# Kernel optimization log

Hardware: AMD Instinct MI355X
Metric: run time of the kernel (lower is better)

## Reference

```python
import jax, jax.numpy as jnp
import numpy as np

T = 16384  # sequence length (scan axis)
D = 512    # d_model


def setup_inputs() -> dict:
    key = jax.random.key(0)
    k1, k2, k3, k4 = jax.random.split(key, 4)
    inputs = jax.random.normal(k1, (T, D), dtype=jnp.float32)
    terminations = jax.random.bernoulli(k2, 0.01, (T,))
    c0 = jnp.zeros((D,), dtype=jnp.float32)
    h0 = jnp.zeros((D,), dtype=jnp.float32)
    # flax OptimizedLSTMCell fuses the 4 gates (order i, f, g, o) into one kernel
    scale = 1.0 / np.sqrt(D).astype(np.float32)
    Wx = jax.random.normal(k3, (D, 4 * D), dtype=jnp.float32) * scale  # input kernel (no bias in flax)
    Wh = jax.random.normal(k4, (D, 4 * D), dtype=jnp.float32) * scale  # recurrent kernel
    b = jnp.zeros((4 * D,), dtype=jnp.float32)                          # recurrent-dense bias
    return {"inputs": inputs, "terminations": terminations, "c0": c0, "h0": h0,
            "Wx": Wx, "Wh": Wh, "b": b}


def reference(inputs, terminations, c0, h0, Wx, Wh, b):
    def step(carry, xt):
        x, term = xt
        c, h = carry
        # reset_on_terminate: zero the carry when this step begins a new episode
        keep = jnp.where(term, jnp.zeros((), c.dtype), jnp.ones((), c.dtype))
        c = c * keep
        h = h * keep
        # fused gate pre-activations, flax gate order: i, f, g, o
        z = x @ Wx + h @ Wh + b  # [4*D]
        i, f, g, o = jnp.split(z, 4, axis=-1)
        new_c = jax.nn.sigmoid(f) * c + jax.nn.sigmoid(i) * jnp.tanh(g)
        new_h = jax.nn.sigmoid(o) * jnp.tanh(new_c)
        return (new_c, new_h), (new_c, new_h)

    _, (cs, hs) = jax.lax.scan(step, (c0, h0), (inputs, terminations))
    # original returns (y_t, new_states) with y_t == new_h per step -> (hs, (cs, hs))
    return hs, cs, hs
```

## Files before the change

kernel.cpp:

```cpp
#include <hip/hip_runtime.h>

typedef _Float16 half8 __attribute__((ext_vector_type(8)));
typedef float floatx4 __attribute__((ext_vector_type(4)));
typedef unsigned int u32x4 __attribute__((ext_vector_type(4)));
typedef unsigned long long u64;
typedef unsigned int u32;
typedef unsigned short u16;

#define T_LEN 16384
#define DM 512
#define NC 2048
#define NG 16
#define NR 16
#define WPG 16
#define WVG 32
#define PROBE_ROUNDS 12
#define PROBE_CAP 4000

struct Meta { int S; int use_h0; int steps_g[NG]; };

union FragU { u64 q[2]; u32x4 r; half8 v; };

__device__ __forceinline__ float sigf(float x) { return 1.0f / (1.0f + __expf(-x)); }
__device__ __forceinline__ float tanh_f(float x) { return 1.0f - 2.0f / (__expf(2.0f * x) + 1.0f); }

__global__ void zero_kernel(u32* __restrict__ p, size_t nwords) {
    size_t i = (size_t)blockIdx.x * blockDim.x + threadIdx.x;
    size_t stride = (size_t)gridDim.x * blockDim.x;
    for (; i < nwords; i += stride) p[i] = 0u;
}

__global__ void pack_f16_kernel(const float* __restrict__ src, _Float16* __restrict__ dst, int n8) {
    int i = blockIdx.x * blockDim.x + threadIdx.x;
    if (i >= n8) return;
    const floatx4* s = (const floatx4*)src + (size_t)i * 2;
    floatx4 a = s[0], b = s[1];
    half8 o;
    o[0] = (_Float16)a[0]; o[1] = (_Float16)a[1]; o[2] = (_Float16)a[2]; o[3] = (_Float16)a[3];
    o[4] = (_Float16)b[0]; o[5] = (_Float16)b[1]; o[6] = (_Float16)b[2]; o[7] = (_Float16)b[3];
    ((half8*)dst)[i] = o;
}

__global__ __launch_bounds__(256) void pack_w_kernel(const float* __restrict__ src, half8* __restrict__ dst) {
    int wid = blockIdx.x * 4 + (threadIdx.x >> 6);
    int l = threadIdx.x & 63;
    int tt = wid >> 4, kt = wid & 15;
    int q = tt & 3, cch = tt >> 2;
    int col = q * 512 + cch * 16 + (l & 15);
    int h = l >> 4;
    half8 o;
#pragma unroll
    for (int jj = 0; jj < 8; jj++) o[jj] = (_Float16)src[(size_t)(kt * 32 + h * 8 + jj) * NC + col];
    dst[(tt * 16 + kt) * 64 + l] = o;
}

__global__ void prep_kernel(const void* __restrict__ termraw, const float* __restrict__ h0,
                            int* __restrict__ seg_start, int* __restrict__ seg_len,
                            Meta* __restrict__ meta, _Float16* __restrict__ Hbuf) {
    __shared__ int cnts[256], offs[256];
    __shared__ int nzm, oddnz, totS;
    __shared__ int chain[256];
    int tid = threadIdx.x;
    if (tid == 0) { nzm = 0; oddnz = 0; }
    __syncthreads();
    const unsigned char* tb = (const unsigned char*)termraw;
    const int* ti = (const int*)termraw;
    int lm = 0;
    for (int i = tid; i < T_LEN; i += 256) {
        if (tb[i]) {
            int p = i & 3;
            if (p == 1 || p == 2) lm |= 1;
            else if (p == 3) lm |= 2;
            else lm |= 4;
        }
    }
    if (lm) atomicOr(&nzm, lm);
    __syncthreads();
    int mm = nzm;
    int bytemode = (mm & 1) ? 1 : 0;
    int floatmode = (!bytemode && (mm & 2)) ? 1 : 0;
    int lo = 0;
    if (!bytemode && !floatmode) {
        for (int k2 = 2 * tid + 1; k2 < T_LEN; k2 += 512) if (ti[k2]) lo = 1;
    }
    if (lo) atomicOr(&oddnz, 1);
    __syncthreads();
    int i64mode = (!bytemode && !floatmode && oddnz == 0 && (mm & 4)) ? 1 : 0;
    const float* tf = (const float*)termraw;

    auto termAt = [&](int t) -> int {
        if (bytemode) return tb[t] != 0;
        if (floatmode) return tf[t] != 0.0f;
        if (i64mode) return (ti[2 * t] != 0) || (ti[2 * t + 1] != 0);
        return ti[t] != 0;
    };

    int base = tid * 64;
    int cnt = 0;
    for (int k = 0; k < 64; k++) {
        int t = base + k;
        if (t == 0 || termAt(t)) cnt++;
    }
    cnts[tid] = cnt;
    __syncthreads();
    if (tid == 0) {
        int a = 0;
        for (int i = 0; i < 256; i++) { offs[i] = a; a += cnts[i]; }
        totS = a;
        meta->S = a;
    }
    __syncthreads();
    int S = totS;
    {
        int o = offs[tid];
        for (int k = 0; k < 64; k++) {
            int t = base + k;
            if (t == 0 || termAt(t)) seg_start[o++] = t;
        }
    }
    __syncthreads();
    for (int i = tid; i < S; i += 256)
        seg_len[i] = ((i + 1 < S) ? seg_start[i + 1] : T_LEN) - seg_start[i];
    __syncthreads();
    {
        int g = tid >> 4, r = tid & 15;
        int tot = 0;
        for (int i = g + 16 * r; i < S; i += 256) tot += seg_len[i];
        chain[tid] = tot;
    }
    __syncthreads();
    if (tid < NG) {
        int mx = 0;
        for (int r = 0; r < 16; r++) mx = max(mx, chain[tid * 16 + r]);
        meta->steps_g[tid] = mx;
    }
    int u = termAt(0);
    if (tid == 0) meta->use_h0 = !u;
    if (!u) {
        for (int d2 = tid; d2 < DM; d2 += 256)
            Hbuf[(d2 >> 3) * 128 + (d2 & 7)] = (_Float16)h0[d2];
    }
}

__global__ __launch_bounds__(256) void xw_gemm_kernel(const half8* __restrict__ A, const half8* __restrict__ B,
                                                      const float* __restrict__ bias, _Float16* __restrict__ XW) {
    int bx = blockIdx.x, by = blockIdx.y;
    int w = threadIdx.x >> 6, l = threadIdx.x & 63;
    int mbase = bx * 64 + w * 16;
    int h = l >> 4, n = l & 15;
    floatx4 acc[8] = {};
    int arow = mbase + n;
#pragma unroll
    for (int kt = 0; kt < 16; kt++) {
        half8 a = A[(size_t)arow * 64 + kt * 4 + h];
#pragma unroll
        for (int nt = 0; nt < 8; nt++)
            acc[nt] = __builtin_amdgcn_mfma_f32_16x16x32_f16(a, B[((by * 8 + nt) * 16 + kt) * 64 + l], acc[nt], 0, 0, 0);
    }
#pragma unroll
    for (int nt = 0; nt < 8; nt++) {
        int tt = by * 8 + nt, q = tt & 3, cch = tt >> 2;
        float bv = bias[q * 512 + cch * 16 + n];
#pragma unroll
        for (int r = 0; r < 4; r++) {
            int row = mbase + h * 4 + r;
            XW[(size_t)row * NC + tt * 16 + n] = (_Float16)(acc[nt][r] + bv);
        }
    }
}

struct Trk { int seg, t0, s0, end, active; };

__device__ __forceinline__ void trk_init(Trk& k, int row, int g, int S,
                                         const int* __restrict__ ss, const int* __restrict__ sl) {
    int seg = g + 16 * row;
    k.seg = seg;
    if (seg < S) { k.t0 = ss[seg]; k.s0 = 0; k.end = sl[seg]; k.active = 1; }
    else { k.t0 = 0; k.s0 = 0; k.end = 0x7fffffff; k.active = 0; }
}

__device__ __forceinline__ int trk_step(Trk& k, int s, int S,
                                        const int* __restrict__ ss, const int* __restrict__ sl, int& t_out) {
    int z = !k.active;
    if (s > 0 && k.active && s == k.end) {
        int seg = k.seg + 256;
        if (seg < S) { k.seg = seg; k.t0 = ss[seg]; k.s0 = s; k.end = s + sl[seg]; z = 1; }
        else { k.active = 0; z = 1; }
    }
    t_out = k.active ? (k.t0 + (s - k.s0)) : 0;
    return z;
}

template <bool L2C>
__device__ __forceinline__ void run_compute(
    const half8* __restrict__ PW, const _Float16* __restrict__ XW,
    const float* __restrict__ c0,
    const int* __restrict__ seg_start, const int* __restrict__ seg_len,
    u64* __restrict__ Hbuf, int* __restrict__ flags,
    int g, int jj, int w, int l, int steps, int S, int use_h0,
    u16 (&hstage)[2][NR][16], _Float16 (&xwstage)[2][NR][128],
    float (&outstage)[2][2][NR][32], int (&ioflag)[2], int (&outcnt)[2]) {
    const int c = jj * 2 + w;
    const int n = l & 15, h = l >> 4;
    const int d = c * 16 + n;
    const int m = n;

    half8 bf[4][16];
#pragma unroll
    for (int q = 0; q < 4; q++)
#pragma unroll
        for (int kt = 0; kt < 16; kt++) {
            bf[q][kt] = PW[((c * 4 + q) * 16 + kt) * 64 + l];
            asm volatile("" : "+v"(bf[q][kt]));
        }

    Trk trkM; trk_init(trkM, n, g, S, seg_start, seg_len);
    Trk trk[4];
#pragma unroll
    for (int r = 0; r < 4; r++) trk_init(trk[r], h * 4 + r, g, S, seg_start, seg_len);

    float cc[4];
#pragma unroll
    for (int r = 0; r < 4; r++) {
        int row = h * 4 + r;
        cc[r] = (g == 0 && row == 0 && use_h0) ? c0[d] : 0.0f;
    }

    FragU zu; zu.q[0] = 0; zu.q[1] = 0;
    const half8 zfrag = zu.v;

    int* fl = flags + g * WVG;
    const int wfid = jj * 2 + w;
    const int pollidx = l & 31;

    const int b2 = l >> 5, m2 = (l >> 1) & 15, half = l & 1;
    const int ktc = c >> 1, hhp = (c & 1) * 2 + b2;
    const int ldsIdx = m2 * 4 + b2 * 2 + half;
    const size_t hwIdx = (size_t)(ktc * 4 + hhp) * 32 + m2 * 2 + half;

    for (int s = 0; s < steps; ++s) {
        int tdump;
        const int zM = trk_step(trkM, s, S, seg_start, seg_len, tdump);
        int zz[4];
#pragma unroll
        for (int r = 0; r < 4; r++)
            zz[r] = trk_step(trk[r], s, S, seg_start, seg_len, tdump);

        while (__hip_atomic_load(&ioflag[s & 1], __ATOMIC_RELAXED, __HIP_MEMORY_SCOPE_WORKGROUP) < s)
            __builtin_amdgcn_s_sleep(1);
        asm volatile("" ::: "memory");
        float xwv[4][4];
#pragma unroll
        for (int q = 0; q < 4; q++)
#pragma unroll
            for (int r = 0; r < 4; r++)
                xwv[q][r] = (float)xwstage[s & 1][h * 4 + r][w * 64 + q * 16 + n];

        if (s > 0) {
            if constexpr (L2C) {
                const int* flp = &fl[pollidx];
                while (true) {
                    int v;
                    asm volatile("global_load_dword %0, %1, off sc0" : "=v"(v) : "v"(flp) : "memory");
                    asm volatile("s_waitcnt vmcnt(0)" ::: "memory");
                    if (__all(v >= s)) break;
                    __builtin_amdgcn_s_sleep(1);
                }
                asm volatile("" ::: "memory");
            } else {
                while (true) {
                    int v = __hip_atomic_load(&fl[pollidx], __ATOMIC_RELAXED, __HIP_MEMORY_SCOPE_AGENT);
                    if (__all(v >= s)) break;
                    __builtin_amdgcn_s_sleep(1);
                }
                asm volatile("" ::: "memory");
            }
        }

        const int rp = s & 1;
        u64* Hr = Hbuf + (size_t)(g * 2 + rp) * (NR * DM / 4);
        u64* Hw = Hbuf + (size_t)(g * 2 + (rp ^ 1)) * (NR * DM / 4);

        u32x4 raw[16];
#pragma unroll
        for (int kt = 0; kt < 16; kt++) {
            const void* ap = (const char*)Hr + (((size_t)kt * 64 + h * 16 + m) << 4);
            if constexpr (L2C)
                asm volatile("global_load_dwordx4 %0, %1, off sc0" : "=v"(raw[kt]) : "v"(ap) : "memory");
            else
                asm volatile("global_load_dwordx4 %0, %1, off sc1" : "=v"(raw[kt]) : "v"(ap) : "memory");
        }
        asm volatile("s_waitcnt vmcnt(0)" ::: "memory");
        __builtin_amdgcn_sched_barrier(0);
        half8 afr[16];
#pragma unroll
        for (int kt = 0; kt < 16; kt++) {
            FragU u; u.r = raw[kt];
            afr[kt] = zM ? zfrag : u.v;
        }

        floatx4 acc[4] = {};
#pragma unroll
        for (int kt = 0; kt < 16; kt++) {
#pragma unroll
            for (int q = 0; q < 4; q++)
                acc[q] = __builtin_amdgcn_mfma_f32_16x16x32_f16(afr[kt], bf[q][kt], acc[q], 0, 0, 0);
        }

        float hnv[4], cnv[4];
#pragma unroll
        for (int r = 0; r < 4; r++) {
            float zi = acc[0][r] + xwv[0][r];
            float zf = acc[1][r] + xwv[1][r];
            float zg = acc[2][r] + xwv[2][r];
            float zo = acc[3][r] + xwv[3][r];
            float cprev = zz[r] ? 0.0f : cc[r];
            float cn = sigf(zf) * cprev + sigf(zi) * tanh_f(zg);
            float hn = sigf(zo) * tanh_f(cn);
            cc[r] = cn; hnv[r] = hn; cnv[r] = cn;
            hstage[w][h * 4 + r][n] = __builtin_bit_cast(u16, (_Float16)hn);
        }

        asm volatile("s_waitcnt lgkmcnt(0)" ::: "memory");
        __builtin_amdgcn_sched_barrier(0);
        u64 pk = ((const u64*)&hstage[w][0][0])[ldsIdx];
        if constexpr (L2C) {
            u64* hwp = &Hw[hwIdx];
            asm volatile("global_store_dwordx2 %0, %1, off sc0" :: "v"(hwp), "v"(pk) : "memory");
        } else {
            __hip_atomic_store(&Hw[hwIdx], pk, __ATOMIC_RELAXED, __HIP_MEMORY_SCOPE_AGENT);
        }

        asm volatile("s_waitcnt vmcnt(0)" ::: "memory");
        if (l == 0) {
            int sp1 = s + 1;
            if constexpr (L2C) {
                int* flw = &fl[wfid];
                asm volatile("global_store_dword %0, %1, off sc0" :: "v"(flw), "v"(sp1) : "memory");
            } else {
                __hip_atomic_store(&fl[wfid], sp1, __ATOMIC_RELAXED, __HIP_MEMORY_SCOPE_AGENT);
            }
        }

        while (__hip_atomic_load(&outcnt[s & 1], __ATOMIC_RELAXED, __HIP_MEMORY_SCOPE_WORKGROUP) == 2)
            __builtin_amdgcn_s_sleep(1);
        asm volatile("" ::: "memory");
#pragma unroll
        for (int r = 0; r < 4; r++) {
            outstage[s & 1][0][h * 4 + r][w * 16 + n] = hnv[r];
            outstage[s & 1][1][h * 4 + r][w * 16 + n] = cnv[r];
        }
        asm volatile("s_waitcnt lgkmcnt(0)" ::: "memory");
        if (l == 0)
            __hip_atomic_fetch_add(&outcnt[s & 1], 1, __ATOMIC_RELAXED, __HIP_MEMORY_SCOPE_WORKGROUP);
    }
}

__global__ __launch_bounds__(192, 1) void scan_kernel(
    const half8* __restrict__ PW, const _Float16* __restrict__ XW,
    const float* __restrict__ c0,
    const int* __restrict__ seg_start, const int* __restrict__ seg_len,
    const Meta* __restrict__ meta,
    u64* __restrict__ Hbuf, int* __restrict__ flags,
    u32* __restrict__ probebuf, int* __restrict__ verdict,
    float* __restrict__ out) {
    const int b = blockIdx.x;
    const int g = (b & 7) * 2 + (b >> 7);
    const int jj = (b >> 3) & 15;
    const int tid = threadIdx.x;
    const int w = tid >> 6, l = tid & 63;
    const int S = meta->S;
    const int steps = meta->steps_g[g];
    if (steps <= 0) return;
    const int use_h0 = meta->use_h0;

    __shared__ __align__(16) u16 hstage[2][NR][16];
    __shared__ __align__(16) _Float16 xwstage[2][NR][128];
    __shared__ __align__(16) float outstage[2][2][NR][32];
    __shared__ int ioflag[2];
    __shared__ int outcnt[2];
    __shared__ int sh_l2ok;

    if (tid == 0) { ioflag[0] = -1; ioflag[1] = -1; outcnt[0] = 0; outcnt[1] = 0; }

    if (w == 0) {
        int okflag = 1;
        u32* pb = probebuf + g * 64;
        for (int r = 0; r < PROBE_ROUNDS && okflag; ++r) {
            u32 tok = 0x10000u | ((u32)r << 8) | (u32)jj;
            if (l == 0) {
                u32* tp = pb + jj;
                asm volatile("global_store_dword %0, %1, off sc0" :: "v"(tp), "v"(tok) : "memory");
                asm volatile("s_waitcnt vmcnt(0)" ::: "memory");
            }
            u32 want = 0x10000u | ((u32)r << 8) | (u32)(l & 15);
            const u32* mp = pb + (l & 15);
            int got = 0;
            for (int it = 0; it < PROBE_CAP; ++it) {
                u32 tv;
                asm volatile("global_load_dword %0, %1, off sc0" : "=v"(tv) : "v"(mp) : "memory");
                asm volatile("s_waitcnt vmcnt(0)" ::: "memory");
                if (__all(tv >= want)) { got = 1; break; }
                __builtin_amdgcn_s_sleep(1);
            }
            if (!got) okflag = 0;
        }
        if (l == 0)
            __hip_atomic_store(&verdict[g * 16 + jj], okflag ? 2 : 1, __ATOMIC_RELAXED, __HIP_MEMORY_SCOPE_AGENT);
        int vv;
        while (true) {
            vv = __hip_atomic_load(&verdict[g * 16 + (l & 15)], __ATOMIC_RELAXED, __HIP_MEMORY_SCOPE_AGENT);
            if (__all(vv != 0)) break;
            __builtin_amdgcn_s_sleep(1);
        }
        if (l == 0) sh_l2ok = __all(vv == 2) ? 1 : 0;
    }
    __syncthreads();
    const int l2ok = sh_l2ok;

    float* outH = out;
    float* outC = out + (size_t)T_LEN * DM;
    float* outH2 = out + 2 * (size_t)T_LEN * DM;

    if (w < 2) {
        if (l2ok)
            run_compute<true>(PW, XW, c0, seg_start, seg_len, Hbuf, flags,
                              g, jj, w, l, steps, S, use_h0,
                              hstage, xwstage, outstage, ioflag, outcnt);
        else
            run_compute<false>(PW, XW, c0, seg_start, seg_len, Hbuf, flags,
                               g, jj, w, l, steps, S, use_h0,
                               hstage, xwstage, outstage, ioflag, outcnt);
    } else {
        const int rX = l >> 4;
        const int rO = l >> 3;
        Trk trkX[4];
#pragma unroll
        for (int i = 0; i < 4; i++) trk_init(trkX[i], rX + 4 * i, g, S, seg_start, seg_len);
        Trk trkO[2];
        trk_init(trkO[0], rO, g, S, seg_start, seg_len);
        trk_init(trkO[1], rO + 8, g, S, seg_start, seg_len);

        auto stageXW = [&](int step, int buf) {
            int tX[4];
#pragma unroll
            for (int i = 0; i < 4; i++) (void)trk_step(trkX[i], step, S, seg_start, seg_len, tX[i]);
            u32x4 xr[4];
#pragma unroll
            for (int i = 0; i < 4; i++)
                xr[i] = *(const u32x4*)((const char*)XW + ((size_t)tX[i] * NC + jj * 128 + (l & 15) * 8) * 2);
#pragma unroll
            for (int i = 0; i < 4; i++)
                *(u32x4*)&xwstage[buf][rX + 4 * i][(l & 15) * 8] = xr[i];
            asm volatile("s_waitcnt lgkmcnt(0)" ::: "memory");
            if (l == 0)
                __hip_atomic_store(&ioflag[buf], step, __ATOMIC_RELAXED, __HIP_MEMORY_SCOPE_WORKGROUP);
        };

        stageXW(0, 0);
        stageXW(1, 1);

        for (int s = 0; s < steps; ++s) {
            int tO[2], aO[2];
#pragma unroll
            for (int j2 = 0; j2 < 2; j2++) {
                (void)trk_step(trkO[j2], s, S, seg_start, seg_len, tO[j2]);
                aO[j2] = trkO[j2].active;
            }
            while (__hip_atomic_load(&outcnt[s & 1], __ATOMIC_RELAXED, __HIP_MEMORY_SCOPE_WORKGROUP) < 2)
                __builtin_amdgcn_s_sleep(1);
            asm volatile("" ::: "memory");
            floatx4 hv[2], cv[2];
#pragma unroll
            for (int j2 = 0; j2 < 2; j2++) {
                hv[j2] = *(floatx4*)&outstage[s & 1][0][rO + 8 * j2][(l & 7) * 4];
                cv[j2] = *(floatx4*)&outstage[s & 1][1][rO + 8 * j2][(l & 7) * 4];
            }
            asm volatile("s_waitcnt lgkmcnt(0)" ::: "memory");
            __hip_atomic_store(&outcnt[s & 1], 0, __ATOMIC_RELAXED, __HIP_MEMORY_SCOPE_WORKGROUP);
#pragma unroll
            for (int j2 = 0; j2 < 2; j2++) {
                if (aO[j2]) {
                    size_t base = (size_t)tO[j2] * DM + jj * 32 + (l & 7) * 4;
                    *(floatx4*)&outH[base] = hv[j2];
                    *(floatx4*)&outC[base] = cv[j2];
                    *(floatx4*)&outH2[base] = hv[j2];
                }
            }
            stageXW(s + 2, s & 1);
        }
    }
}

extern "C" void kernel_launch(void* const* d_in, const int* in_sizes, int n_in,
                              void* d_out, int out_size, void* d_ws, size_t ws_size,
                              hipStream_t stream) {
    const float* inputs = (const float*)d_in[0];
    const void* terms = d_in[1];
    const float* c0 = (const float*)d_in[2];
    const float* h0 = (const float*)d_in[3];
    const float* Wx = (const float*)d_in[4];
    const float* Wh = (const float*)d_in[5];
    const float* bias = (const float*)d_in[6];
    float* out = (float*)d_out;

    size_t off = 0;
    auto take = [&](size_t bts) { size_t cur = off; off = (off + bts + 255) & ~(size_t)255; return cur; };
    size_t offXW = take((size_t)T_LEN * NC * 2);
    size_t offAin = take((size_t)T_LEN * DM * 2);
    size_t offPX = take((size_t)DM * NC * 2);
    size_t offPW = take((size_t)DM * NC * 2);
    size_t offSS = take((size_t)(T_LEN + 2) * 4);
    size_t offSL = take((size_t)(T_LEN + 2) * 4);
    size_t offH = take(2ull * NG * NR * DM * 2);
    size_t offFL = take((size_t)NG * WVG * 4);
    size_t offPB = take((size_t)NG * 256);
    size_t offVD = take((size_t)NG * WPG * 4);
    size_t offME = take(256);
    size_t total = off;
    (void)ws_size;

    char* W = (char*)d_ws;
    _Float16* Ain = (_Float16*)(W + offAin);
    half8* PX = (half8*)(W + offPX);
    half8* PWp = (half8*)(W + offPW);
    int* segS = (int*)(W + offSS);
    int* segL = (int*)(W + offSL);
    Meta* meta = (Meta*)(W + offME);
    _Float16* XWp = (_Float16*)(W + offXW);

    size_t zwords = (total - offH) / 4;
    zero_kernel<<<256, 256, 0, stream>>>((u32*)(W + offH), zwords);
    pack_f16_kernel<<<(T_LEN * DM / 8 + 255) / 256, 256, 0, stream>>>(inputs, Ain, T_LEN * DM / 8);
    pack_w_kernel<<<512, 256, 0, stream>>>(Wx, PX);
    pack_w_kernel<<<512, 256, 0, stream>>>(Wh, PWp);
    prep_kernel<<<1, 256, 0, stream>>>(terms, h0, segS, segL, meta, (_Float16*)(W + offH));

    dim3 gg(T_LEN / 64, NC / 128);
    xw_gemm_kernel<<<gg, 256, 0, stream>>>((const half8*)Ain, (const half8*)PX, bias, XWp);
    scan_kernel<<<256, 192, 0, stream>>>((const half8*)PWp, XWp, c0, segS, segL, meta,
                                         (u64*)(W + offH), (int*)(W + offFL),
                                         (u32*)(W + offPB), (int*)(W + offVD), out);
}
```

Measured before the change: 2.215 ms.

## Assign scan groups to workgroups by their actual XCD placement

Each workgroup reads its XCC id from a hardware register and publishes it. Block 0 then builds a mapping so that each 16-block group lands on a single XCD where possible, which lets those groups use the fast L2-coherent path. Groups that cannot be co-located skip the L2 probe entirely, and the probe rounds and spin cap are reduced. The cost is a grid-wide handshake through block 0 at kernel start, which relies on all 256 blocks being co-resident.

```diff
diff --git a/kernel.cpp b/kernel.cpp
--- a/kernel.cpp
+++ b/kernel.cpp
@@ -14,8 +14,8 @@
 #define NR 16
 #define WPG 16
 #define WVG 32
-#define PROBE_ROUNDS 12
-#define PROBE_CAP 4000
+#define PROBE_ROUNDS 6
+#define PROBE_CAP 1200
 
 struct Meta { int S; int use_h0; int steps_g[NG]; };
 
@@ -363,15 +363,12 @@
     const Meta* __restrict__ meta,
     u64* __restrict__ Hbuf, int* __restrict__ flags,
     u32* __restrict__ probebuf, int* __restrict__ verdict,
+    int* __restrict__ xcdbuf, int* __restrict__ asg,
     float* __restrict__ out) {
     const int b = blockIdx.x;
-    const int g = (b & 7) * 2 + (b >> 7);
-    const int jj = (b >> 3) & 15;
     const int tid = threadIdx.x;
     const int w = tid >> 6, l = tid & 63;
     const int S = meta->S;
-    const int steps = meta->steps_g[g];
-    if (steps <= 0) return;
     const int use_h0 = meta->use_h0;
 
     __shared__ __align__(16) u16 hstage[2][NR][16];
@@ -379,31 +376,78 @@
     __shared__ __align__(16) float outstage[2][2][NR][32];
     __shared__ int ioflag[2];
     __shared__ int outcnt[2];
+    __shared__ int sh_asg;
     __shared__ int sh_l2ok;
 
     if (tid == 0) { ioflag[0] = -1; ioflag[1] = -1; outcnt[0] = 0; outcnt[1] = 0; }
 
+    if (tid == 0) {
+        u32 xcc = __builtin_amdgcn_s_getreg(63508) & 7;
+        __hip_atomic_store(&xcdbuf[b], (int)(xcc + 1), __ATOMIC_RELAXED, __HIP_MEMORY_SCOPE_AGENT);
+    }
+    if (b == 0 && tid == 0) {
+        int cxc[8] = {0, 0, 0, 0, 0, 0, 0, 0};
+        for (int w2 = 0; w2 < 256; ++w2) {
+            int v;
+            while ((v = __hip_atomic_load(&xcdbuf[w2], __ATOMIC_RELAXED, __HIP_MEMORY_SCOPE_AGENT)) == 0)
+                __builtin_amdgcn_s_sleep(1);
+            cxc[(v - 1) & 7]++;
+        }
+        int base_g[8], ng_x[8], gi = 0;
+        for (int x = 0; x < 8; ++x) {
+            int t = cxc[x] >> 4;
+            if (t > NG - gi) t = NG - gi;
+            ng_x[x] = t; base_g[x] = gi; gi += t;
+        }
+        const int lg = gi;
+        int kx[8] = {0, 0, 0, 0, 0, 0, 0, 0};
+        int lk = 0;
+        for (int w2 = 0; w2 < 256; ++w2) {
+            int x = (__hip_atomic_load(&xcdbuf[w2], __ATOMIC_RELAXED, __HIP_MEMORY_SCOPE_AGENT) - 1) & 7;
+            int g2, j2, l2;
+            if (kx[x] < ng_x[x] * 16) {
+                g2 = base_g[x] + (kx[x] >> 4); j2 = kx[x] & 15; l2 = 1; kx[x]++;
+            } else {
+                g2 = lg + (lk >> 4); j2 = lk & 15; l2 = 0; lk++;
+            }
+            __hip_atomic_store(&asg[w2], ((l2 << 8) | (g2 << 4) | j2) + 1,
+                               __ATOMIC_RELAXED, __HIP_MEMORY_SCOPE_AGENT);
+        }
+    }
+    if (tid == 0) {
+        int v;
+        while ((v = __hip_atomic_load(&asg[b], __ATOMIC_RELAXED, __HIP_MEMORY_SCOPE_AGENT)) == 0)
+            __builtin_amdgcn_s_sleep(1);
+        sh_asg = v - 1;
+    }
+    __syncthreads();
+    const int g = (sh_asg >> 4) & 15;
+    const int jj = sh_asg & 15;
+    const int l2cand = (sh_asg >> 8) & 1;
+
     if (w == 0) {
-        int okflag = 1;
-        u32* pb = probebuf + g * 64;
-        for (int r = 0; r < PROBE_ROUNDS && okflag; ++r) {
-            u32 tok = 0x10000u | ((u32)r << 8) | (u32)jj;
-            if (l == 0) {
-                u32* tp = pb + jj;
-                asm volatile("global_store_dword %0, %1, off sc0" :: "v"(tp), "v"(tok) : "memory");
-                asm volatile("s_waitcnt vmcnt(0)" ::: "memory");
-            }
-            u32 want = 0x10000u | ((u32)r << 8) | (u32)(l & 15);
-            const u32* mp = pb + (l & 15);
-            int got = 0;
-            for (int it = 0; it < PROBE_CAP; ++it) {
-                u32 tv;
-                asm volatile("global_load_dword %0, %1, off sc0" : "=v"(tv) : "v"(mp) : "memory");
-                asm volatile("s_waitcnt vmcnt(0)" ::: "memory");
-                if (__all(tv >= want)) { got = 1; break; }
-                __builtin_amdgcn_s_sleep(1);
-            }
-            if (!got) okflag = 0;
+        int okflag = l2cand;
+        if (l2cand) {
+            u32* pb = probebuf + g * 64;
+            for (int r = 0; r < PROBE_ROUNDS && okflag; ++r) {
+                u32 tok = 0x10000u | ((u32)r << 8) | (u32)jj;
+                if (l == 0) {
+                    u32* tp = pb + jj;
+                    asm volatile("global_store_dword %0, %1, off sc0" :: "v"(tp), "v"(tok) : "memory");
+                    asm volatile("s_waitcnt vmcnt(0)" ::: "memory");
+                }
+                u32 want = 0x10000u | ((u32)r << 8) | (u32)(l & 15);
+                const u32* mp = pb + (l & 15);
+                int got = 0;
+                for (int it = 0; it < PROBE_CAP; ++it) {
+                    u32 tv;
+                    asm volatile("global_load_dword %0, %1, off sc0" : "=v"(tv) : "v"(mp) : "memory");
+                    asm volatile("s_waitcnt vmcnt(0)" ::: "memory");
+                    if (__all(tv >= want)) { got = 1; break; }
+                    __builtin_amdgcn_s_sleep(1);
+                }
+                if (!got) okflag = 0;
+            }
         }
         if (l == 0)
             __hip_atomic_store(&verdict[g * 16 + jj], okflag ? 2 : 1, __ATOMIC_RELAXED, __HIP_MEMORY_SCOPE_AGENT);
@@ -417,6 +461,9 @@
     }
     __syncthreads();
     const int l2ok = sh_l2ok;
+
+    const int steps = meta->steps_g[g];
+    if (steps <= 0) return;
 
     float* outH = out;
     float* outC = out + (size_t)T_LEN * DM;
@@ -516,6 +563,8 @@
     size_t offFL = take((size_t)NG * WVG * 4);
     size_t offPB = take((size_t)NG * 256);
     size_t offVD = take((size_t)NG * WPG * 4);
+    size_t offXC = take(256 * 4);
+    size_t offAS = take(256 * 4);
     size_t offME = take(256);
     size_t total = off;
     (void)ws_size;
@@ -540,5 +589,6 @@
     xw_gemm_kernel<<<gg, 256, 0, stream>>>((const half8*)Ain, (const half8*)PX, bias, XWp);
     scan_kernel<<<256, 192, 0, stream>>>((const half8*)PWp, XWp, c0, segS, segL, meta,
                                          (u64*)(W + offH), (int*)(W + offFL),
-                                         (u32*)(W + offPB), (int*)(W + offVD), out);
-}
+                                         (u32*)(W + offPB), (int*)(W + offVD),
+                                         (int*)(W + offXC), (int*)(W + offAS), out);
+}
```

Measured after the change: 2.069 ms. -6.6%, faster.
